# Performance work log

Hardware: AMD Instinct MI355X
Metric: run time of the kernel (lower is better)

The kernel has to match this reference:

```python
import jax, jax.numpy as jnp
import numpy as np

N_QUBITS = 23
DEPTH = 2
ROT_PER_QUBIT = 2
DIM = 1 << N_QUBITS
CYCLE = ('RY', 'RZ', 'RX')
C64 = jnp.complex64


def _rot_mat(kind, theta):
    # standard rotation gates; theta is the full angle, matrices use theta/2
    c = jnp.cos(theta / 2).astype(C64)
    s = jnp.sin(theta / 2).astype(C64)
    if kind == 'RX':
        return jnp.stack([jnp.stack([c, -1j * s]), jnp.stack([-1j * s, c])])
    if kind == 'RY':
        return jnp.stack([jnp.stack([c, -s]), jnp.stack([s, c])])
    # RZ = diag(exp(-i t/2), exp(i t/2))
    z = jnp.zeros((), C64)
    return jnp.stack([jnp.stack([c - 1j * s, z]), jnp.stack([z, c + 1j * s])])


def _apply_1q(psi, mat, q):
    # qubit 0 is the most significant bit -> axis q after factoring
    psi = psi.reshape(1 << q, 2, -1)
    psi = jnp.einsum('ij,ajb->aib', mat, psi)
    return psi.reshape(-1)


def _apply_cnot(psi, c):
    # control c, target c+1 (adjacent): flip target axis where control == 1
    psi = psi.reshape(1 << c, 2, 2, -1)
    psi = jnp.stack([psi[:, 0], psi[:, 1, ::-1]], axis=1)
    return psi.reshape(-1)


def setup_inputs() -> dict:
    key = jax.random.key(0)
    k1, k2, k3 = jax.random.split(key, 3)
    thetas = jax.random.uniform(k1, (DEPTH * N_QUBITS * ROT_PER_QUBIT,), dtype=jnp.float32)
    state_real = jax.random.normal(k2, (DIM,), dtype=jnp.float32)
    state_imag = jax.random.normal(k3, (DIM,), dtype=jnp.float32)
    return {"thetas": thetas, "state_real": state_real, "state_imag": state_imag}


def reference(thetas, state_real, state_imag):
    psi = (state_real + 1j * state_imag).astype(C64)
    psi = psi / jnp.linalg.norm(psi)  # normalized input state
    idx = 0
    for layer in range(DEPTH):
        for q in range(N_QUBITS):
            for r in range(ROT_PER_QUBIT):
                kind = CYCLE[(layer * ROT_PER_QUBIT + r) % 3]
                psi = _apply_1q(psi, _rot_mat(kind, thetas[idx]), q)
                idx += 1
        for q in range(N_QUBITS - 1):
            psi = _apply_cnot(psi, q)
    probs = jnp.abs(psi) ** 2
    # Z on qubit 0 (MSB): eig +1 for first half, -1 for second half
    p = probs.reshape(2, -1)
    return (p[0].sum() - p[1].sum()).astype(jnp.float32)
```

## Files before the change

### kernel.cpp

```cpp
#include <hip/hip_runtime.h>

#define Q21 (1u<<21)
#define THREADS 512
#define BLOCKS 1024


struct cd { double r, i; };
__device__ __forceinline__ cd cmul(cd a, cd b){ return {a.r*b.r - a.i*b.i, a.r*b.i + a.i*b.r}; }
__device__ __forceinline__ cd cjg(cd a){ return {a.r, -a.i}; }
__device__ __forceinline__ cd cadd(cd a, cd b){ return {a.r+b.r, a.i+b.i}; }

__global__ void initk(const float* __restrict__ thetas, float* __restrict__ cmat,
                      double* __restrict__ accum){
  if(threadIdx.x != 0) return;
  accum[0]=0.0; accum[1]=0.0;
  double a0=0.5*(double)thetas[0], b0=0.5*(double)thetas[1];
  double a1=0.5*(double)thetas[2], b1=0.5*(double)thetas[3];
  double ax=0.5*(double)thetas[46], bx=0.5*(double)thetas[47];
  cd U0[2][2], U1[2][2];
  {
    double ca=cos(a0), sa=sin(a0), cb=cos(b0), sb=sin(b0);
    U0[0][0]={ca*cb,-ca*sb}; U0[0][1]={-sa*cb, sa*sb};
    U0[1][0]={sa*cb, sa*sb}; U0[1][1]={ ca*cb, ca*sb};
  }
  {
    double ca=cos(a1), sa=sin(a1), cb=cos(b1), sb=sin(b1);
    U1[0][0]={ca*cb,-ca*sb}; U1[0][1]={-sa*cb, sa*sb};
    U1[1][0]={sa*cb, sa*sb}; U1[1][1]={ ca*cb, ca*sb};
  }
  cd V[2][2];
  {
    double ca=cos(ax), sa=sin(ax), cb=cos(bx), sb=sin(bx);
    V[0][0]={cb*ca, sb*sa}; V[0][1]={-sb*ca,-cb*sa};
    V[1][0]={sb*ca,-cb*sa}; V[1][1]={ cb*ca,-sb*sa};
  }
  double aM = (V[0][0].r*V[0][0].r+V[0][0].i*V[0][0].i)
            - (V[1][0].r*V[1][0].r+V[1][0].i*V[1][0].i);
  cd O01 = cadd(cmul(cjg(V[0][0]),V[0][1]), {-cmul(cjg(V[1][0]),V[1][1]).r,
                                             -cmul(cjg(V[1][0]),V[1][1]).i});
  cd B[4][4];
  for(int j=0;j<4;++j) for(int k=0;k<4;++k) B[j][k]={0,0};
  B[0][0]={aM,0}; B[1][1]={aM,0}; B[2][2]={-aM,0}; B[3][3]={-aM,0};
  B[0][3]=O01; B[3][0]=cjg(O01); B[1][2]=O01; B[2][1]=cjg(O01);
  cd W[4][4];
  for(int m=0;m<4;++m) for(int n=0;n<4;++n)
    W[m][n] = cmul(U0[m>>1][n>>1], U1[m&1][n&1]);
  cd C[4][4];
  for(int m=0;m<4;++m) for(int n=0;n<4;++n){
    cd s={0,0};
    for(int j=0;j<4;++j) for(int k=0;k<4;++k)
      s = cadd(s, cmul(cmul(cjg(W[j][m]), B[j][k]), W[k][n]));
    C[m][n]=s;
  }
  cmat[0]=(float)C[0][0].r; cmat[1]=(float)C[1][1].r;
  cmat[2]=(float)C[2][2].r; cmat[3]=(float)C[3][3].r;
  const int pm[6]={0,0,0,1,1,2}, pn[6]={1,2,3,2,3,3};
  for(int p=0;p<6;++p){
    cmat[4+2*p]   = (float)(2.0*C[pm[p]][pn[p]].r);
    cmat[5+2*p]   = (float)(2.0*C[pm[p]][pn[p]].i);
  }
}

__global__ __launch_bounds__(THREADS)
void mainp(const float* __restrict__ sr, const float* __restrict__ si,
           const float* __restrict__ cmat, double* __restrict__ accum){
  int gt = blockIdx.x*THREADS + threadIdx.x;
  int v  = gt<<2;
  float rr[4][4], ii[4][4];
  *(float4*)&rr[0][0] = *(const float4*)(sr+v);
  *(float4*)&rr[1][0] = *(const float4*)(sr+v+Q21);
  *(float4*)&rr[2][0] = *(const float4*)(sr+v+2*Q21);
  *(float4*)&rr[3][0] = *(const float4*)(sr+v+3*Q21);
  *(float4*)&ii[0][0] = *(const float4*)(si+v);
  *(float4*)&ii[1][0] = *(const float4*)(si+v+Q21);
  *(float4*)&ii[2][0] = *(const float4*)(si+v+2*Q21);
  *(float4*)&ii[3][0] = *(const float4*)(si+v+3*Q21);
  float cm[16];
  #pragma unroll
  for(int k=0;k<16;++k) cm[k]=cmat[k];
  float ssum=0.f, nsum=0.f;
  #pragma unroll
  for(int e=0;e<4;++e){
    float qr[4]={rr[0][e],rr[1][e],rr[2][e],rr[3][e]};
    float qi[4]={ii[0][e],ii[1][e],ii[2][e],ii[3][e]};
    float n0=qr[0]*qr[0]+qi[0]*qi[0], n1=qr[1]*qr[1]+qi[1]*qi[1];
    float n2=qr[2]*qr[2]+qi[2]*qi[2], n3=qr[3]*qr[3]+qi[3]*qi[3];
    nsum += (n0+n1)+(n2+n3);
    float s = cm[0]*n0 + cm[1]*n1 + cm[2]*n2 + cm[3]*n3;
    const int pm[6]={0,0,0,1,1,2}, pn[6]={1,2,3,2,3,3};
    #pragma unroll
    for(int p=0;p<6;++p){
      int m=pm[p], n=pn[p];
      float zr = qr[m]*qr[n] + qi[m]*qi[n];
      float zi = qr[m]*qi[n] - qi[m]*qr[n];
      s += cm[4+2*p]*zr - cm[5+2*p]*zi;
    }
    ssum += s;
  }
  double ds=(double)ssum, dn=(double)nsum;
  #pragma unroll
  for(int off=32;off>0;off>>=1){ ds += __shfl_down(ds,off); dn += __shfl_down(dn,off); }
  __shared__ double red[16];
  int w = threadIdx.x>>6;
  if((threadIdx.x&63)==0){ red[w]=ds; red[8+w]=dn; }
  __syncthreads();
  if(threadIdx.x==0){
    double s=0,n=0;
    #pragma unroll
    for(int i=0;i<8;++i){ s+=red[i]; n+=red[8+i]; }
    atomicAdd(accum+1, s); atomicAdd(accum+0, n);
  }
}

__global__ void fink(const double* __restrict__ accum, float* __restrict__ out){
  out[0] = (float)(accum[1]/accum[0]);
}

extern "C" void kernel_launch(void* const* d_in, const int* in_sizes, int n_in,
                              void* d_out, int out_size, void* d_ws, size_t ws_size,
                              hipStream_t stream){
  (void)in_sizes; (void)n_in; (void)out_size; (void)ws_size;
  const float* thetas = (const float*)d_in[0];
  const float* sr = (const float*)d_in[1];
  const float* si = (const float*)d_in[2];
  char* ws = (char*)d_ws;
  double* accum = (double*)ws;
  float* cmat = (float*)(ws + 64);

  initk<<<1, 64, 0, stream>>>(thetas, cmat, accum);
  mainp<<<BLOCKS, THREADS, 0, stream>>>(sr, si, cmat, accum);
  fink<<<1, 1, 0, stream>>>(accum, (float*)d_out);
}
```

Baseline: 120.0 us.

## Accumulate Gram-matrix entries, defer theta-dependent contraction to final kernel

The main kernel now accumulates the 16 real components of the 4x4 Gram matrix of the top-two-qubit amplitudes, independent of the angles. The serial initk launch that built the coefficient matrix is removed, and that math moves into the final reduction kernel, which contracts the reduced Gram matrix with C. Global atomics are replaced by per-block partial writes. In exchange, the main kernel does 16 wave shuffle reductions per step instead of 2 and has higher register pressure.

Result: slower. 126.3 us (+5.3%).

```diff
diff --git a/kernel.cpp b/kernel.cpp
--- a/kernel.cpp
+++ b/kernel.cpp
@@ -10,60 +10,9 @@
 __device__ __forceinline__ cd cjg(cd a){ return {a.r, -a.i}; }
 __device__ __forceinline__ cd cadd(cd a, cd b){ return {a.r+b.r, a.i+b.i}; }
 
-__global__ void initk(const float* __restrict__ thetas, float* __restrict__ cmat,
-                      double* __restrict__ accum){
-  if(threadIdx.x != 0) return;
-  accum[0]=0.0; accum[1]=0.0;
-  double a0=0.5*(double)thetas[0], b0=0.5*(double)thetas[1];
-  double a1=0.5*(double)thetas[2], b1=0.5*(double)thetas[3];
-  double ax=0.5*(double)thetas[46], bx=0.5*(double)thetas[47];
-  cd U0[2][2], U1[2][2];
-  {
-    double ca=cos(a0), sa=sin(a0), cb=cos(b0), sb=sin(b0);
-    U0[0][0]={ca*cb,-ca*sb}; U0[0][1]={-sa*cb, sa*sb};
-    U0[1][0]={sa*cb, sa*sb}; U0[1][1]={ ca*cb, ca*sb};
-  }
-  {
-    double ca=cos(a1), sa=sin(a1), cb=cos(b1), sb=sin(b1);
-    U1[0][0]={ca*cb,-ca*sb}; U1[0][1]={-sa*cb, sa*sb};
-    U1[1][0]={sa*cb, sa*sb}; U1[1][1]={ ca*cb, ca*sb};
-  }
-  cd V[2][2];
-  {
-    double ca=cos(ax), sa=sin(ax), cb=cos(bx), sb=sin(bx);
-    V[0][0]={cb*ca, sb*sa}; V[0][1]={-sb*ca,-cb*sa};
-    V[1][0]={sb*ca,-cb*sa}; V[1][1]={ cb*ca,-sb*sa};
-  }
-  double aM = (V[0][0].r*V[0][0].r+V[0][0].i*V[0][0].i)
-            - (V[1][0].r*V[1][0].r+V[1][0].i*V[1][0].i);
-  cd O01 = cadd(cmul(cjg(V[0][0]),V[0][1]), {-cmul(cjg(V[1][0]),V[1][1]).r,
-                                             -cmul(cjg(V[1][0]),V[1][1]).i});
-  cd B[4][4];
-  for(int j=0;j<4;++j) for(int k=0;k<4;++k) B[j][k]={0,0};
-  B[0][0]={aM,0}; B[1][1]={aM,0}; B[2][2]={-aM,0}; B[3][3]={-aM,0};
-  B[0][3]=O01; B[3][0]=cjg(O01); B[1][2]=O01; B[2][1]=cjg(O01);
-  cd W[4][4];
-  for(int m=0;m<4;++m) for(int n=0;n<4;++n)
-    W[m][n] = cmul(U0[m>>1][n>>1], U1[m&1][n&1]);
-  cd C[4][4];
-  for(int m=0;m<4;++m) for(int n=0;n<4;++n){
-    cd s={0,0};
-    for(int j=0;j<4;++j) for(int k=0;k<4;++k)
-      s = cadd(s, cmul(cmul(cjg(W[j][m]), B[j][k]), W[k][n]));
-    C[m][n]=s;
-  }
-  cmat[0]=(float)C[0][0].r; cmat[1]=(float)C[1][1].r;
-  cmat[2]=(float)C[2][2].r; cmat[3]=(float)C[3][3].r;
-  const int pm[6]={0,0,0,1,1,2}, pn[6]={1,2,3,2,3,3};
-  for(int p=0;p<6;++p){
-    cmat[4+2*p]   = (float)(2.0*C[pm[p]][pn[p]].r);
-    cmat[5+2*p]   = (float)(2.0*C[pm[p]][pn[p]].i);
-  }
-}
-
 __global__ __launch_bounds__(THREADS)
-void mainp(const float* __restrict__ sr, const float* __restrict__ si,
-           const float* __restrict__ cmat, double* __restrict__ accum){
+void gramk(const float* __restrict__ sr, const float* __restrict__ si,
+           double* __restrict__ part){
   int gt = blockIdx.x*THREADS + threadIdx.x;
   int v  = gt<<2;
   float rr[4][4], ii[4][4];
@@ -75,45 +24,108 @@
   *(float4*)&ii[1][0] = *(const float4*)(si+v+Q21);
   *(float4*)&ii[2][0] = *(const float4*)(si+v+2*Q21);
   *(float4*)&ii[3][0] = *(const float4*)(si+v+3*Q21);
-  float cm[16];
+  float acc[16];
   #pragma unroll
-  for(int k=0;k<16;++k) cm[k]=cmat[k];
-  float ssum=0.f, nsum=0.f;
+  for(int k=0;k<16;++k) acc[k]=0.f;
+  const int pm[6]={0,0,0,1,1,2}, pn[6]={1,2,3,2,3,3};
   #pragma unroll
   for(int e=0;e<4;++e){
     float qr[4]={rr[0][e],rr[1][e],rr[2][e],rr[3][e]};
     float qi[4]={ii[0][e],ii[1][e],ii[2][e],ii[3][e]};
-    float n0=qr[0]*qr[0]+qi[0]*qi[0], n1=qr[1]*qr[1]+qi[1]*qi[1];
-    float n2=qr[2]*qr[2]+qi[2]*qi[2], n3=qr[3]*qr[3]+qi[3]*qi[3];
-    nsum += (n0+n1)+(n2+n3);
-    float s = cm[0]*n0 + cm[1]*n1 + cm[2]*n2 + cm[3]*n3;
-    const int pm[6]={0,0,0,1,1,2}, pn[6]={1,2,3,2,3,3};
+    #pragma unroll
+    for(int m=0;m<4;++m) acc[m] += qr[m]*qr[m] + qi[m]*qi[m];
     #pragma unroll
     for(int p=0;p<6;++p){
       int m=pm[p], n=pn[p];
-      float zr = qr[m]*qr[n] + qi[m]*qi[n];
-      float zi = qr[m]*qi[n] - qi[m]*qr[n];
-      s += cm[4+2*p]*zr - cm[5+2*p]*zi;
+      acc[4+2*p] += qr[m]*qr[n] + qi[m]*qi[n];
+      acc[5+2*p] += qr[m]*qi[n] - qi[m]*qr[n];
     }
-    ssum += s;
   }
-  double ds=(double)ssum, dn=(double)nsum;
+  double d[16];
   #pragma unroll
-  for(int off=32;off>0;off>>=1){ ds += __shfl_down(ds,off); dn += __shfl_down(dn,off); }
-  __shared__ double red[16];
+  for(int k=0;k<16;++k) d[k]=(double)acc[k];
+  #pragma unroll
+  for(int off=32;off>0;off>>=1){
+    #pragma unroll
+    for(int k=0;k<16;++k) d[k] += __shfl_down(d[k], off);
+  }
+  __shared__ double red[8][16];
   int w = threadIdx.x>>6;
-  if((threadIdx.x&63)==0){ red[w]=ds; red[8+w]=dn; }
+  if((threadIdx.x&63)==0){
+    #pragma unroll
+    for(int k=0;k<16;++k) red[w][k]=d[k];
+  }
   __syncthreads();
-  if(threadIdx.x==0){
-    double s=0,n=0;
+  if(threadIdx.x<16){
+    double s=0;
     #pragma unroll
-    for(int i=0;i<8;++i){ s+=red[i]; n+=red[8+i]; }
-    atomicAdd(accum+1, s); atomicAdd(accum+0, n);
+    for(int i=0;i<8;++i) s += red[i][threadIdx.x];
+    part[blockIdx.x*16 + threadIdx.x] = s;
   }
 }
 
-__global__ void fink(const double* __restrict__ accum, float* __restrict__ out){
-  out[0] = (float)(accum[1]/accum[0]);
+__global__ void fink(const float* __restrict__ thetas,
+                     const double* __restrict__ part, float* __restrict__ out){
+  __shared__ double red[16][17];
+  __shared__ double G[16];
+  int t = threadIdx.x;
+  int comp = t&15, grp = t>>4;
+  double s = 0.0;
+  for(int b=grp; b<BLOCKS; b+=16) s += part[b*16 + comp];
+  red[comp][grp] = s;
+  __syncthreads();
+  if(t<16){
+    double g=0;
+    #pragma unroll
+    for(int i=0;i<16;++i) g += red[t][i];
+    G[t]=g;
+  }
+  __syncthreads();
+  if(t==0){
+    double a0=0.5*(double)thetas[0], b0=0.5*(double)thetas[1];
+    double a1=0.5*(double)thetas[2], b1=0.5*(double)thetas[3];
+    double ax=0.5*(double)thetas[46], bx=0.5*(double)thetas[47];
+    cd U0[2][2], U1[2][2], V[2][2];
+    {
+      double ca=cos(a0), sa=sin(a0), cb=cos(b0), sb=sin(b0);
+      U0[0][0]={ca*cb,-ca*sb}; U0[0][1]={-sa*cb, sa*sb};
+      U0[1][0]={sa*cb, sa*sb}; U0[1][1]={ ca*cb, ca*sb};
+    }
+    {
+      double ca=cos(a1), sa=sin(a1), cb=cos(b1), sb=sin(b1);
+      U1[0][0]={ca*cb,-ca*sb}; U1[0][1]={-sa*cb, sa*sb};
+      U1[1][0]={sa*cb, sa*sb}; U1[1][1]={ ca*cb, ca*sb};
+    }
+    {
+      double ca=cos(ax), sa=sin(ax), cb=cos(bx), sb=sin(bx);
+      V[0][0]={cb*ca, sb*sa}; V[0][1]={-sb*ca,-cb*sa};
+      V[1][0]={sb*ca,-cb*sa}; V[1][1]={ cb*ca,-sb*sa};
+    }
+    double aM = (V[0][0].r*V[0][0].r+V[0][0].i*V[0][0].i)
+              - (V[1][0].r*V[1][0].r+V[1][0].i*V[1][0].i);
+    cd O01 = cadd(cmul(cjg(V[0][0]),V[0][1]), {-cmul(cjg(V[1][0]),V[1][1]).r,
+                                               -cmul(cjg(V[1][0]),V[1][1]).i});
+    cd B[4][4];
+    for(int j=0;j<4;++j) for(int k=0;k<4;++k) B[j][k]={0,0};
+    B[0][0]={aM,0}; B[1][1]={aM,0}; B[2][2]={-aM,0}; B[3][3]={-aM,0};
+    B[0][3]=O01; B[3][0]=cjg(O01); B[1][2]=O01; B[2][1]=cjg(O01);
+    cd W[4][4];
+    for(int m=0;m<4;++m) for(int n=0;n<4;++n)
+      W[m][n] = cmul(U0[m>>1][n>>1], U1[m&1][n&1]);
+    cd C[4][4];
+    for(int m=0;m<4;++m) for(int n=0;n<4;++n){
+      cd sacc={0,0};
+      for(int j=0;j<4;++j) for(int k=0;k<4;++k)
+        sacc = cadd(sacc, cmul(cmul(cjg(W[j][m]), B[j][k]), W[k][n]));
+      C[m][n]=sacc;
+    }
+    const int pm[6]={0,0,0,1,1,2}, pn[6]={1,2,3,2,3,3};
+    double num = C[0][0].r*G[0] + C[1][1].r*G[1] + C[2][2].r*G[2] + C[3][3].r*G[3];
+    for(int p=0;p<6;++p)
+      num += 2.0*C[pm[p]][pn[p]].r*G[4+2*p] - 2.0*C[pm[p]][pn[p]].i*G[5+2*p];
+    double den = G[0]+G[1]+G[2]+G[3];
+    out[0] = (float)(num/den);
+  }
 }
 
 extern "C" void kernel_launch(void* const* d_in, const int* in_sizes, int n_in,
@@ -123,11 +135,8 @@
   const float* thetas = (const float*)d_in[0];
   const float* sr = (const float*)d_in[1];
   const float* si = (const float*)d_in[2];
-  char* ws = (char*)d_ws;
-  double* accum = (double*)ws;
-  float* cmat = (float*)(ws + 64);
+  double* part = (double*)d_ws;
 
-  initk<<<1, 64, 0, stream>>>(thetas, cmat, accum);
-  mainp<<<BLOCKS, THREADS, 0, stream>>>(sr, si, cmat, accum);
-  fink<<<1, 1, 0, stream>>>(accum, (float*)d_out);
+  gramk<<<BLOCKS, THREADS, 0, stream>>>(sr, si, part);
+  fink<<<1, 256, 0, stream>>>(thetas, part, (float*)d_out);
 }
```
